# Kernel optimization log

Hardware: AMD Instinct MI355X
Metric: run time of the kernel (lower is better)

Reference implementation:

```python
import jax, jax.numpy as jnp
import numpy as np

VOL = (32, 64, 64)          # 3D brain volume grid
B, N, D = 2, 4096, 1024     # batch, active voxels (seq_len), feature_dim
H, KNN = 16, 16             # num_heads, num_neighbors


def setup_inputs() -> dict:
    key = jax.random.key(0)
    k1, k2, k3, k4 = jax.random.split(key, 4)
    # boolean 3D mask with exactly N active voxels (so seq_len == #active)
    rng = np.random.default_rng(0)
    flat = np.zeros(int(np.prod(VOL)), dtype=bool)
    flat[rng.choice(flat.size, N, replace=False)] = True
    visual_cortex_mask = jnp.asarray(flat.reshape(VOL))
    x = jax.random.normal(k1, (B, N, D), dtype=jnp.float32)
    s = 1.0 / np.sqrt(D)
    Wq = jax.random.normal(k2, (D, D), dtype=jnp.float32) * s
    Wk = jax.random.normal(k3, (D, D), dtype=jnp.float32) * s
    Wv = jax.random.normal(k4, (D, D), dtype=jnp.float32) * s
    return {"x": x, "visual_cortex_mask": visual_cortex_mask,
            "Wq": Wq, "Wk": Wk, "Wv": Wv}


def reference(x, visual_cortex_mask, Wq, Wk, Wv):
    batch, seq_len, d = x.shape
    hd = d // H
    # --- kNN over active voxel coordinates (cdist + topk) ---
    flat = visual_cortex_mask.reshape(-1)
    (act,) = jnp.nonzero(flat, size=seq_len)  # flat indices of active voxels
    coords = jnp.stack(jnp.unravel_index(act, visual_cortex_mask.shape),
                       axis=1).astype(jnp.float32)           # [N, 3]
    sq = jnp.sum(coords * coords, axis=-1)                    # [N]
    d2 = sq[:, None] + sq[None, :] - 2.0 * (coords @ coords.T)  # squared dists
    _, nbr = jax.lax.top_k(-d2, KNN + 1)   # smallest distances first
    nbr = nbr[:, 1:]                       # drop self -> [N, KNN] positions
    # --- QKV projections (torch Linear: x @ W.T) ---
    q = (x @ Wq.T).reshape(batch, seq_len, H, hd)
    k = (x @ Wk.T).reshape(batch, seq_len, H, hd)
    v = (x @ Wv.T).reshape(batch, seq_len, H, hd)
    # --- gather-based sparse attention: each query attends only to its
    # KNN neighbors (exactly the block-mask semantics of the original) ---
    kn = k[:, nbr]   # [B, N, KNN, H, hd]
    vn = v[:, nbr]   # [B, N, KNN, H, hd]
    scale = 1.0 / np.sqrt(hd)
    scores = jnp.einsum('bnhd,bnkhd->bhnk', q, kn) * scale
    attn = jax.nn.softmax(scores, axis=-1)
    out = jnp.einsum('bhnk,bnkhd->bnhd', attn, vn).reshape(batch, seq_len, d)
    metric = k.mean(axis=2)  # key.mean over heads -> [B, N, hd]
    return out, metric
```

## Files before the change

### kernel.cpp

```cpp
#include <hip/hip_runtime.h>
#include <hip/hip_bf16.h>
#include <stdint.h>

#define BATCH 2
#define NPTS 4096
#define DMODEL 1024
#define NHEAD 16
#define HDIM 64
#define KNN 16
#define MASKN 131072
#define EBLK 128

typedef __attribute__((ext_vector_type(8))) short bf16x8;
typedef __attribute__((ext_vector_type(4))) float f32x4;

__device__ __forceinline__ float b2f(unsigned short u) {
    union { unsigned int i; float f; } c; c.i = ((unsigned int)u) << 16; return c.f;
}
__device__ __forceinline__ unsigned short f2b(float f) {
    unsigned int x = __float_as_uint(f);
    unsigned int r = (x + 0x7fffu + ((x >> 16) & 1u)) >> 16;
    return (unsigned short)r;
}
__device__ __forceinline__ unsigned int pack2f(float a, float b) {
    return (unsigned int)f2b(a) | ((unsigned int)f2b(b) << 16);
}
__device__ __forceinline__ void gload16(const unsigned short* g, unsigned short* l) {
    __builtin_amdgcn_global_load_lds((const __attribute__((address_space(1))) void*)g,
                                     (__attribute__((address_space(3))) void*)l, 16, 0, 0);
}

__global__ __launch_bounds__(256) void count8_kernel(const unsigned char* __restrict__ m8,
                                                     int* __restrict__ cnt8) {
    __shared__ int red[256];
    const int b = blockIdx.x, t = threadIdx.x;
    const uchar4 v = ((const uchar4*)m8)[b * 256 + t];
    red[t] = (v.x != 0) + (v.y != 0) + (v.z != 0) + (v.w != 0);
    __syncthreads();
    for (int off = 128; off >= 1; off >>= 1) {
        if (t < off) red[t] += red[t + off];
        __syncthreads();
    }
    if (t == 0) cnt8[b] = red[0];
}

__global__ __launch_bounds__(256) void count32_kernel(const unsigned char* __restrict__ m8,
                                                      const int* __restrict__ cnt8,
                                                      int* __restrict__ cnt32) {
    __shared__ int red[256];
    const int b = blockIdx.x, t = threadIdx.x;
    red[t] = (t < EBLK) ? cnt8[t] : 0;
    __syncthreads();
    for (int off = 128; off >= 1; off >>= 1) {
        if (t < off) red[t] += red[t + off];
        __syncthreads();
    }
    if (red[0] == NPTS) return;
    __syncthreads();
    const int4 v = ((const int4*)m8)[b * 256 + t];
    red[t] = (v.x != 0) + (v.y != 0) + (v.z != 0) + (v.w != 0);
    __syncthreads();
    for (int off = 128; off >= 1; off >>= 1) {
        if (t < off) red[t] += red[t + off];
        __syncthreads();
    }
    if (t == 0) cnt32[b] = red[0];
}

__global__ __launch_bounds__(256) void extract_kernel(const unsigned char* __restrict__ m8,
                                                      const int* __restrict__ cnt8,
                                                      const int* __restrict__ cnt32,
                                                      int* __restrict__ act) {
    __shared__ int sblk[EBLK];
    __shared__ int sthr[256];
    const int b = blockIdx.x, t = threadIdx.x;
    if (t < EBLK) sblk[t] = cnt8[t];
    __syncthreads();
    for (int off = 1; off < EBLK; off <<= 1) {
        int v = (t < EBLK && t >= off) ? sblk[t - off] : 0;
        __syncthreads();
        if (t < EBLK) sblk[t] += v;
        __syncthreads();
    }
    const bool bytes = (sblk[EBLK - 1] == NPTS);
    if (!bytes) {
        __syncthreads();
        if (t < EBLK) sblk[t] = cnt32[t];
        __syncthreads();
        for (int off = 1; off < EBLK; off <<= 1) {
            int v = (t < EBLK && t >= off) ? sblk[t - off] : 0;
            __syncthreads();
            if (t < EBLK) sblk[t] += v;
            __syncthreads();
        }
    }
    const int blkoff = (b == 0) ? 0 : sblk[b - 1];
    const int gbase = b * 1024 + t * 4;
    int f0, f1, f2, f3;
    if (bytes) {
        const uchar4 v = ((const uchar4*)m8)[b * 256 + t];
        f0 = v.x != 0; f1 = v.y != 0; f2 = v.z != 0; f3 = v.w != 0;
    } else {
        const int4 v = ((const int4*)m8)[b * 256 + t];
        f0 = v.x != 0; f1 = v.y != 0; f2 = v.z != 0; f3 = v.w != 0;
    }
    const int c = f0 + f1 + f2 + f3;
    sthr[t] = c;
    __syncthreads();
    for (int off = 1; off < 256; off <<= 1) {
        int v = (t >= off) ? sthr[t - off] : 0;
        __syncthreads();
        sthr[t] += v;
        __syncthreads();
    }
    int pos = blkoff + sthr[t] - c;
    if (f0) act[pos++] = gbase;
    if (f1) act[pos++] = gbase + 1;
    if (f2) act[pos++] = gbase + 2;
    if (f3) act[pos++] = gbase + 3;
}

#define XN8 (BATCH * NPTS * DMODEL / 8)
#define WN8 (DMODEL * DMODEL / 8)
#define CASTN (XN8 + 3 * WN8)
#define CASTBLKS ((CASTN + 255) / 256)

__global__ __launch_bounds__(256) void knn_cast_kernel(
    const int* __restrict__ act, int* __restrict__ nbr,
    const float* __restrict__ x, const float* __restrict__ wq,
    const float* __restrict__ wk, const float* __restrict__ wv,
    unsigned short* __restrict__ Xb, unsigned short* __restrict__ Wb)
{
    __shared__ int act_s[NPTS];
    const int t = threadIdx.x;
    if (blockIdx.x < 1024) {
        for (int i = t; i < NPTS; i += 256) act_s[i] = act[i];
        __syncthreads();
        const int q = blockIdx.x * 4 + (t >> 6);
        const int lane = t & 63;
        const int aq = act_s[q];
        const int qz = aq >> 12, qy = (aq >> 6) & 63, qx = aq & 63;
        int best[17];
        #pragma unroll
        for (int i = 0; i < 17; ++i) best[i] = 0x7FFFFFFF;
        for (int j = lane; j < NPTS; j += 64) {
            const int aj = act_s[j];
            const int dz = (aj >> 12) - qz;
            const int dy = ((aj >> 6) & 63) - qy;
            const int dx = (aj & 63) - qx;
            const int d2 = dz * dz + dy * dy + dx * dx;
            int p = (d2 << 12) | j;
            if (p < best[16]) {
                #pragma unroll
                for (int u = 0; u < 17; ++u) {
                    const bool lt = p < best[u];
                    const int tmp = best[u];
                    best[u] = lt ? p : best[u];
                    p = lt ? tmp : p;
                }
            }
        }
        int head = best[0];
        int keep = 0;
        #pragma unroll
        for (int r = 0; r < KNN + 1; ++r) {
            int m = head;
            #pragma unroll
            for (int off = 32; off >= 1; off >>= 1) m = min(m, __shfl_xor(m, off, 64));
            if (lane == r - 1) keep = m;
            const bool win = (head == m);
            #pragma unroll
            for (int u = 0; u < 16; ++u) if (win) best[u] = best[u + 1];
            if (win) best[16] = 0x7FFFFFFF;
            head = best[0];
        }
        if (lane < KNN) nbr[q * KNN + lane] = keep & 4095;
    } else {
        const int i = (blockIdx.x - 1024) * 256 + t;
        if (i >= CASTN) return;
        const float* src;
        unsigned short* dst;
        if (i < XN8) {
            src = x + (size_t)i * 8;
            dst = Xb + (size_t)i * 8;
        } else {
            const int j = i - XN8;
            const int wsel = j >> 17;
            const int o = j & (WN8 - 1);
            src = ((wsel == 0) ? wq : (wsel == 1) ? wk : wv) + (size_t)o * 8;
            dst = Wb + ((size_t)wsel * WN8 + o) * 8;
        }
        const float4 a = ((const float4*)src)[0];
        const float4 bb = ((const float4*)src)[1];
        uint4 w;
        w.x = pack2f(a.x, a.y);  w.y = pack2f(a.z, a.w);
        w.z = pack2f(bb.x, bb.y); w.w = pack2f(bb.z, bb.w);
        *(uint4*)dst = w;
    }
}

__global__ __launch_bounds__(256, 2) void gemm_qkv64(
    const unsigned short* __restrict__ Xb,
    const unsigned short* __restrict__ Wb,
    unsigned short* __restrict__ O0, unsigned short* __restrict__ O1, unsigned short* __restrict__ O2)
{
    const int K = DMODEL, N = DMODEL;
    const unsigned short* W = Wb + (size_t)blockIdx.z * DMODEL * DMODEL;
    unsigned short* C = (blockIdx.z == 0) ? O0 : (blockIdx.z == 1) ? O1 : O2;
    __shared__ unsigned short As[2][128 * 64];
    __shared__ unsigned short Bs[2][128 * 64];
    const int tid = threadIdx.x;
    const int rowBase = blockIdx.x * 128;
    const int colBase = blockIdx.y * 128;
    const int lane = tid & 63, w = tid >> 6;
    const int wr = w >> 1, wc = w & 1;
    const int lr = lane & 15, kg = lane >> 4;

    f32x4 acc[4][4];
    const f32x4 zero = {0.f, 0.f, 0.f, 0.f};
    #pragma unroll
    for (int i = 0; i < 4; ++i)
        #pragma unroll
        for (int j = 0; j < 4; ++j) acc[i][j] = zero;

    const unsigned short* aS[4];
    const unsigned short* bS[4];
    #pragma unroll
    for (int j = 0; j < 4; ++j) {
        const int s = j * 256 + tid;
        const int row = s >> 3, pch = s & 7;
        const int sc = (pch ^ (row & 7)) * 8;
        aS[j] = Xb + (size_t)(rowBase + row) * K + sc;
        bS[j] = W  + (size_t)(colBase + row) * K + sc;
    }

    #define STAGE(kt, bf) do { \
        _Pragma("unroll") \
        for (int j = 0; j < 4; ++j) { \
            gload16(aS[j] + (kt) * 64, &As[bf][(j * 256 + w * 64) * 8]); \
            gload16(bS[j] + (kt) * 64, &Bs[bf][(j * 256 + w * 64) * 8]); \
        } \
    } while (0)

    #define COMPUTE(bf) do { \
        bf16x8 af[4][2], bfr[4][2]; \
        _Pragma("unroll") \
        for (int mi = 0; mi < 4; ++mi) \
            _Pragma("unroll") \
            for (int kk = 0; kk < 2; ++kk) \
                af[mi][kk] = *(const bf16x8*)&As[bf][(wr * 64 + mi * 16 + lr) * 64 + (((kk * 4 + kg) ^ (lr & 7)) * 8)]; \
        _Pragma("unroll") \
        for (int ni = 0; ni < 4; ++ni) \
            _Pragma("unroll") \
            for (int kk = 0; kk < 2; ++kk) \
                bfr[ni][kk] = *(const bf16x8*)&Bs[bf][(wc * 64 + ni * 16 + lr) * 64 + (((kk * 4 + kg) ^ (lr & 7)) * 8)]; \
        __builtin_amdgcn_s_setprio(1); \
        _Pragma("unroll") \
        for (int kk = 0; kk < 2; ++kk) \
            _Pragma("unroll") \
            for (int mi = 0; mi < 4; ++mi) \
                _Pragma("unroll") \
                for (int ni = 0; ni < 4; ++ni) \
                    acc[mi][ni] = __builtin_amdgcn_mfma_f32_16x16x32_bf16(af[mi][kk], bfr[ni][kk], acc[mi][ni], 0, 0, 0); \
        __builtin_amdgcn_s_setprio(0); \
    } while (0)

    STAGE(0, 0);
    STAGE(1, 1);
    for (int kt = 0; kt < 14; ++kt) {
        const int bf = kt & 1;
        asm volatile("s_waitcnt vmcnt(8)" ::: "memory");
        __builtin_amdgcn_s_barrier();
        COMPUTE(bf);
        __builtin_amdgcn_s_barrier();
        STAGE(kt + 2, bf);
    }
    asm volatile("s_waitcnt vmcnt(8)" ::: "memory");
    __builtin_amdgcn_s_barrier();
    COMPUTE(0);
    __builtin_amdgcn_s_barrier();
    asm volatile("s_waitcnt vmcnt(0)" ::: "memory");
    __builtin_amdgcn_s_barrier();
    COMPUTE(1);
    #undef STAGE
    #undef COMPUTE

    #pragma unroll
    for (int mi = 0; mi < 4; ++mi)
        #pragma unroll
        for (int ni = 0; ni < 4; ++ni) {
            const int row0 = rowBase + wr * 64 + mi * 16 + kg * 4;
            const int col = colBase + wc * 64 + ni * 16 + lr;
            #pragma unroll
            for (int j = 0; j < 4; ++j)
                C[(size_t)(row0 + j) * N + col] = f2b(acc[mi][ni][j]);
        }
}

__device__ __forceinline__ void stage16(unsigned short* dst, const float* src) {
    const float4 a = ((const float4*)src)[0];
    const float4 b = ((const float4*)src)[1];
    const float4 c = ((const float4*)src)[2];
    const float4 d = ((const float4*)src)[3];
    uint4 w0, w1;
    w0.x = pack2f(a.x, a.y); w0.y = pack2f(a.z, a.w);
    w0.z = pack2f(b.x, b.y); w0.w = pack2f(b.z, b.w);
    w1.x = pack2f(c.x, c.y); w1.y = pack2f(c.z, c.w);
    w1.z = pack2f(d.x, d.y); w1.w = pack2f(d.z, d.w);
    ((uint4*)dst)[0] = w0;
    ((uint4*)dst)[1] = w1;
}

__global__ __launch_bounds__(256) void gemm_qkv_f32(
    const float* __restrict__ X,
    const float* __restrict__ W0, const float* __restrict__ W1, const float* __restrict__ W2,
    unsigned short* __restrict__ O0, unsigned short* __restrict__ O1, unsigned short* __restrict__ O2)
{
    const int K = DMODEL, N = DMODEL;
    const float* W = (blockIdx.z == 0) ? W0 : (blockIdx.z == 1) ? W1 : W2;
    unsigned short* C = (blockIdx.z == 0) ? O0 : (blockIdx.z == 1) ? O1 : O2;
    __shared__ unsigned short As[128 * 32];
    __shared__ unsigned short Bs[128 * 32];
    const int tid = threadIdx.x;
    const int rowBase = blockIdx.x * 128;
    const int colBase = blockIdx.y * 128;
    const int lane = tid & 63, w = tid >> 6;
    const int wr = w >> 1, wc = w & 1;
    const int lr = lane & 15, kg = lane >> 4;
    const int srow = tid >> 1;
    const int scol = (tid & 1) * 16;
    f32x4 acc[4][4];
    const f32x4 zero = {0.f, 0.f, 0.f, 0.f};
    #pragma unroll
    for (int i = 0; i < 4; ++i)
        #pragma unroll
        for (int j = 0; j < 4; ++j) acc[i][j] = zero;
    const float* Arow = &X[(size_t)(rowBase + srow) * K + scol];
    const float* Brow = &W[(size_t)(colBase + srow) * K + scol];
    unsigned short* Adst = &As[srow * 32 + scol];
    unsigned short* Bdst = &Bs[srow * 32 + scol];
    for (int kb = 0; kb < K; kb += 32) {
        __syncthreads();
        stage16(Adst, Arow + kb);
        stage16(Bdst, Brow + kb);
        __syncthreads();
        bf16x8 af[4], bfr[4];
        #pragma unroll
        for (int mi = 0; mi < 4; ++mi)
            af[mi] = *(const bf16x8*)&As[(wr * 64 + mi * 16 + lr) * 32 + kg * 8];
        #pragma unroll
        for (int ni = 0; ni < 4; ++ni)
            bfr[ni] = *(const bf16x8*)&Bs[(wc * 64 + ni * 16 + lr) * 32 + kg * 8];
        #pragma unroll
        for (int mi = 0; mi < 4; ++mi)
            #pragma unroll
            for (int ni = 0; ni < 4; ++ni)
                acc[mi][ni] = __builtin_amdgcn_mfma_f32_16x16x32_bf16(af[mi], bfr[ni], acc[mi][ni], 0, 0, 0);
    }
    #pragma unroll
    for (int mi = 0; mi < 4; ++mi)
        #pragma unroll
        for (int ni = 0; ni < 4; ++ni) {
            const int row0 = rowBase + wr * 64 + mi * 16 + kg * 4;
            const int col = colBase + wc * 64 + ni * 16 + lr;
            #pragma unroll
            for (int j = 0; j < 4; ++j)
                C[(size_t)(row0 + j) * N + col] = f2b(acc[mi][ni][j]);
        }
}

__global__ __launch_bounds__(256) void attn_kernel(
    const unsigned short* __restrict__ Q, const unsigned short* __restrict__ Kb,
    const unsigned short* __restrict__ Vb, const int* __restrict__ nbr,
    float* __restrict__ out, float* __restrict__ mout)
{
    const int bid = blockIdx.x;
    const int p = (bid & 7) * 1024 + (bid >> 3);
    const int b = p >> 12;
    const int n = p & 4095;
    __shared__ unsigned short q_s[DMODEL];
    __shared__ float a_s[NHEAD][KNN];
    __shared__ float part_s[4][64];
    const int tid = threadIdx.x;
    const int kk = tid & 15, h = tid >> 4;
    const int mynb = nbr[n * KNN + kk];
    const unsigned short* krow = &Kb[((size_t)b * NPTS + mynb) * DMODEL + h * HDIM];
    bf16x8 kreg[8];
    #pragma unroll
    for (int j = 0; j < 8; ++j) kreg[j] = *(const bf16x8*)&krow[j * 8];
    const int o = tid * 4;
    ushort4 vpre[KNN];
    #pragma unroll
    for (int k2 = 0; k2 < KNN; ++k2) {
        const int nb2 = __shfl(mynb, k2, 16);
        vpre[k2] = *(const ushort4*)&Vb[((size_t)b * NPTS + nb2) * DMODEL + o];
    }
    *(int2*)&q_s[tid * 4] = *(const int2*)&Q[((size_t)b * NPTS + n) * DMODEL + tid * 4];
    __syncthreads();
    float s = 0.f;
    #pragma unroll
    for (int j = 0; j < 8; ++j) {
        const bf16x8 qq = *(const bf16x8*)&q_s[h * HDIM + j * 8];
        const bf16x8 kr = kreg[j];
        #pragma unroll
        for (int e = 0; e < 8; ++e)
            s += b2f((unsigned short)qq[e]) * b2f((unsigned short)kr[e]);
    }
    s *= 0.125f;
    float m = s;
    #pragma unroll
    for (int off = 8; off >= 1; off >>= 1) m = fmaxf(m, __shfl_xor(m, off, 16));
    const float e = __expf(s - m);
    float sum = e;
    #pragma unroll
    for (int off = 8; off >= 1; off >>= 1) sum += __shfl_xor(sum, off, 16);
    a_s[h][kk] = e / sum;
    __syncthreads();
    const int h2 = tid >> 4;
    float av0 = 0.f, av1 = 0.f, av2 = 0.f, av3 = 0.f;
    #pragma unroll
    for (int k2 = 0; k2 < KNN; ++k2) {
        const float a = a_s[h2][k2];
        av0 += a * b2f(vpre[k2].x); av1 += a * b2f(vpre[k2].y);
        av2 += a * b2f(vpre[k2].z); av3 += a * b2f(vpre[k2].w);
    }
    float4 r; r.x = av0; r.y = av1; r.z = av2; r.w = av3;
    *(float4*)&out[((size_t)b * NPTS + n) * DMODEL + o] = r;
    {
        const unsigned short* krow2 = &Kb[((size_t)b * NPTS + n) * DMODEL];
        const int dd = tid & 63, grp = tid >> 6;
        float ms = 0.f;
        #pragma unroll
        for (int hh = 0; hh < 4; ++hh)
            ms += b2f(krow2[(grp * 4 + hh) * HDIM + dd]);
        part_s[grp][dd] = ms;
        __syncthreads();
        if (tid < 64)
            mout[((size_t)b * NPTS + n) * HDIM + tid] =
                (part_s[0][tid] + part_s[1][tid] + part_s[2][tid] + part_s[3][tid]) * 0.0625f;
    }
}

extern "C" void kernel_launch(void* const* d_in, const int* in_sizes, int n_in,
                              void* d_out, int out_size, void* d_ws, size_t ws_size,
                              hipStream_t stream) {
    const float* x = (const float*)d_in[0];
    const unsigned char* mask = (const unsigned char*)d_in[1];
    const float* Wq = (const float*)d_in[2];
    const float* Wk = (const float*)d_in[3];
    const float* Wv = (const float*)d_in[4];
    float* out = (float*)d_out;
    char* ws = (char*)d_ws;

    const size_t QKV_BYTES = (size_t)BATCH * NPTS * DMODEL * 2;
    const size_t XB_BYTES  = (size_t)BATCH * NPTS * DMODEL * 2;
    const size_t WB_BYTES  = (size_t)3 * DMODEL * DMODEL * 2;
    unsigned short* qb = (unsigned short*)(ws);
    unsigned short* kb = (unsigned short*)(ws + QKV_BYTES);
    unsigned short* vb = (unsigned short*)(ws + 2 * QKV_BYTES);
    const size_t SMALL_BYTES = (size_t)NPTS * sizeof(int) * (1 + KNN) + 2 * EBLK * sizeof(int);
    const size_t need_base = 3 * QKV_BYTES + SMALL_BYTES;
    const size_t need_full = need_base + XB_BYTES + WB_BYTES;
    const bool full = (ws_size >= need_full);
    char* tail = ws + 3 * QKV_BYTES;
    unsigned short* Xb = (unsigned short*)tail;
    unsigned short* Wb = (unsigned short*)(tail + XB_BYTES);
    char* small = full ? (tail + XB_BYTES + WB_BYTES) : tail;
    int* act  = (int*)small;
    int* nbr  = (int*)(small + NPTS * sizeof(int));
    int* cnt8 = (int*)(small + NPTS * sizeof(int) * (1 + KNN));
    int* cnt32 = cnt8 + EBLK;
    if (ws_size < need_base) return;

    count8_kernel<<<EBLK, 256, 0, stream>>>(mask, cnt8);
    count32_kernel<<<EBLK, 256, 0, stream>>>(mask, cnt8, cnt32);
    extract_kernel<<<EBLK, 256, 0, stream>>>(mask, cnt8, cnt32, act);
    if (full) {
        knn_cast_kernel<<<1024 + CASTBLKS, 256, 0, stream>>>(act, nbr, x, Wq, Wk, Wv, Xb, Wb);
        gemm_qkv64<<<dim3(64, 8, 3), 256, 0, stream>>>(Xb, Wb, qb, kb, vb);
    } else {
        knn_cast_kernel<<<1024, 256, 0, stream>>>(act, nbr, x, Wq, Wk, Wv,
                                                  (unsigned short*)nullptr, (unsigned short*)nullptr);
        gemm_qkv_f32<<<dim3(64, 8, 3), 256, 0, stream>>>(x, Wq, Wk, Wv, qb, kb, vb);
    }
    attn_kernel<<<dim3(BATCH * NPTS), 256, 0, stream>>>(qb, kb, vb, nbr, out,
                                                        out + (size_t)BATCH * NPTS * DMODEL);
}
```

Baseline: 167.4 us.

## Fuse bf16 cast into mask count kernel and kNN into QKV GEMM launch

Moves the fp32-to-bf16 cast of x and the weights into the first mask-counting kernel, so the cast runs alongside the count stage. The kNN search is merged into the same launch as the QKV GEMM, so kNN blocks and GEMM tiles can overlap on the GPU and one launch boundary disappears. The cost is that the fused GEMM kernel now also reserves the kNN shared memory (16 KB more per block), which may lower GEMM occupancy. kNN and GEMM blocks also compete for CUs within the same grid.

```diff
diff --git a/kernel.cpp b/kernel.cpp
--- a/kernel.cpp
+++ b/kernel.cpp
@@ -30,18 +30,52 @@
                                      (__attribute__((address_space(3))) void*)l, 16, 0, 0);
 }
 
-__global__ __launch_bounds__(256) void count8_kernel(const unsigned char* __restrict__ m8,
-                                                     int* __restrict__ cnt8) {
+#define XN8 (BATCH * NPTS * DMODEL / 8)
+#define WN8 (DMODEL * DMODEL / 8)
+#define CASTN (XN8 + 3 * WN8)
+#define CASTBLKS ((CASTN + 255) / 256)
+
+__global__ __launch_bounds__(256) void cast_count8_kernel(
+    const float* __restrict__ x, const float* __restrict__ wq,
+    const float* __restrict__ wk, const float* __restrict__ wv,
+    unsigned short* __restrict__ Xb, unsigned short* __restrict__ Wb,
+    const unsigned char* __restrict__ m8, int* __restrict__ cnt8, int do_cast)
+{
     __shared__ int red[256];
-    const int b = blockIdx.x, t = threadIdx.x;
-    const uchar4 v = ((const uchar4*)m8)[b * 256 + t];
-    red[t] = (v.x != 0) + (v.y != 0) + (v.z != 0) + (v.w != 0);
-    __syncthreads();
-    for (int off = 128; off >= 1; off >>= 1) {
-        if (t < off) red[t] += red[t + off];
-        __syncthreads();
-    }
-    if (t == 0) cnt8[b] = red[0];
+    const int t = threadIdx.x;
+    const int cb = do_cast ? CASTBLKS : 0;
+    if ((int)blockIdx.x < cb) {
+        const int i = blockIdx.x * 256 + t;
+        if (i >= CASTN) return;
+        const float* src;
+        unsigned short* dst;
+        if (i < XN8) {
+            src = x + (size_t)i * 8;
+            dst = Xb + (size_t)i * 8;
+        } else {
+            const int j = i - XN8;
+            const int wsel = j >> 17;
+            const int o = j & (WN8 - 1);
+            src = ((wsel == 0) ? wq : (wsel == 1) ? wk : wv) + (size_t)o * 8;
+            dst = Wb + ((size_t)wsel * WN8 + o) * 8;
+        }
+        const float4 a = ((const float4*)src)[0];
+        const float4 bb = ((const float4*)src)[1];
+        uint4 w;
+        w.x = pack2f(a.x, a.y);  w.y = pack2f(a.z, a.w);
+        w.z = pack2f(bb.x, bb.y); w.w = pack2f(bb.z, bb.w);
+        *(uint4*)dst = w;
+    } else {
+        const int b = blockIdx.x - cb;
+        const uchar4 v = ((const uchar4*)m8)[b * 256 + t];
+        red[t] = (v.x != 0) + (v.y != 0) + (v.z != 0) + (v.w != 0);
+        __syncthreads();
+        for (int off = 128; off >= 1; off >>= 1) {
+            if (t < off) red[t] += red[t + off];
+            __syncthreads();
+        }
+        if (t == 0) cnt8[b] = red[0];
+    }
 }
 
 __global__ __launch_bounds__(256) void count32_kernel(const unsigned char* __restrict__ m8,
@@ -120,20 +154,19 @@
     if (f3) act[pos++] = gbase + 3;
 }
 
-#define XN8 (BATCH * NPTS * DMODEL / 8)
-#define WN8 (DMODEL * DMODEL / 8)
-#define CASTN (XN8 + 3 * WN8)
-#define CASTBLKS ((CASTN + 255) / 256)
-
-__global__ __launch_bounds__(256) void knn_cast_kernel(
+__global__ __launch_bounds__(256, 2) void knn_gemm_kernel(
     const int* __restrict__ act, int* __restrict__ nbr,
-    const float* __restrict__ x, const float* __restrict__ wq,
-    const float* __restrict__ wk, const float* __restrict__ wv,
-    unsigned short* __restrict__ Xb, unsigned short* __restrict__ Wb)
+    const unsigned short* __restrict__ Xb,
+    const unsigned short* __restrict__ Wb,
+    unsigned short* __restrict__ O0, unsigned short* __restrict__ O1, unsigned short* __restrict__ O2)
 {
+    __shared__ unsigned short As[2][128 * 64];
+    __shared__ unsigned short Bs[2][128 * 64];
     __shared__ int act_s[NPTS];
-    const int t = threadIdx.x;
-    if (blockIdx.x < 1024) {
+    const int tid = threadIdx.x;
+
+    if ((int)blockIdx.x < 1024) {
+        const int t = tid;
         for (int i = t; i < NPTS; i += 256) act_s[i] = act[i];
         __syncthreads();
         const int q = blockIdx.x * 4 + (t >> 6);
@@ -175,43 +208,18 @@
             head = best[0];
         }
         if (lane < KNN) nbr[q * KNN + lane] = keep & 4095;
-    } else {
-        const int i = (blockIdx.x - 1024) * 256 + t;
-        if (i >= CASTN) return;
-        const float* src;
-        unsigned short* dst;
-        if (i < XN8) {
-            src = x + (size_t)i * 8;
-            dst = Xb + (size_t)i * 8;
-        } else {
-            const int j = i - XN8;
-            const int wsel = j >> 17;
-            const int o = j & (WN8 - 1);
-            src = ((wsel == 0) ? wq : (wsel == 1) ? wk : wv) + (size_t)o * 8;
-            dst = Wb + ((size_t)wsel * WN8 + o) * 8;
-        }
-        const float4 a = ((const float4*)src)[0];
-        const float4 bb = ((const float4*)src)[1];
-        uint4 w;
-        w.x = pack2f(a.x, a.y);  w.y = pack2f(a.z, a.w);
-        w.z = pack2f(bb.x, bb.y); w.w = pack2f(bb.z, bb.w);
-        *(uint4*)dst = w;
-    }
-}
-
-__global__ __launch_bounds__(256, 2) void gemm_qkv64(
-    const unsigned short* __restrict__ Xb,
-    const unsigned short* __restrict__ Wb,
-    unsigned short* __restrict__ O0, unsigned short* __restrict__ O1, unsigned short* __restrict__ O2)
-{
+        return;
+    }
+
+    const int g = blockIdx.x - 1024;
+    const int bx = g & 63;
+    const int by = (g >> 6) & 7;
+    const int bz = g >> 9;
     const int K = DMODEL, N = DMODEL;
-    const unsigned short* W = Wb + (size_t)blockIdx.z * DMODEL * DMODEL;
-    unsigned short* C = (blockIdx.z == 0) ? O0 : (blockIdx.z == 1) ? O1 : O2;
-    __shared__ unsigned short As[2][128 * 64];
-    __shared__ unsigned short Bs[2][128 * 64];
-    const int tid = threadIdx.x;
-    const int rowBase = blockIdx.x * 128;
-    const int colBase = blockIdx.y * 128;
+    const unsigned short* W = Wb + (size_t)bz * DMODEL * DMODEL;
+    unsigned short* C = (bz == 0) ? O0 : (bz == 1) ? O1 : O2;
+    const int rowBase = bx * 128;
+    const int colBase = by * 128;
     const int lane = tid & 63, w = tid >> 6;
     const int wr = w >> 1, wc = w & 1;
     const int lr = lane & 15, kg = lane >> 4;
@@ -297,6 +305,53 @@
         }
 }
 
+__global__ __launch_bounds__(256) void knn_kernel(const int* __restrict__ act,
+                                                  int* __restrict__ nbr) {
+    __shared__ int act_s[NPTS];
+    const int t = threadIdx.x;
+    for (int i = t; i < NPTS; i += 256) act_s[i] = act[i];
+    __syncthreads();
+    const int q = blockIdx.x * 4 + (t >> 6);
+    const int lane = t & 63;
+    const int aq = act_s[q];
+    const int qz = aq >> 12, qy = (aq >> 6) & 63, qx = aq & 63;
+    int best[17];
+    #pragma unroll
+    for (int i = 0; i < 17; ++i) best[i] = 0x7FFFFFFF;
+    for (int j = lane; j < NPTS; j += 64) {
+        const int aj = act_s[j];
+        const int dz = (aj >> 12) - qz;
+        const int dy = ((aj >> 6) & 63) - qy;
+        const int dx = (aj & 63) - qx;
+        const int d2 = dz * dz + dy * dy + dx * dx;
+        int p = (d2 << 12) | j;
+        if (p < best[16]) {
+            #pragma unroll
+            for (int u = 0; u < 17; ++u) {
+                const bool lt = p < best[u];
+                const int tmp = best[u];
+                best[u] = lt ? p : best[u];
+                p = lt ? tmp : p;
+            }
+        }
+    }
+    int head = best[0];
+    int keep = 0;
+    #pragma unroll
+    for (int r = 0; r < KNN + 1; ++r) {
+        int m = head;
+        #pragma unroll
+        for (int off = 32; off >= 1; off >>= 1) m = min(m, __shfl_xor(m, off, 64));
+        if (lane == r - 1) keep = m;
+        const bool win = (head == m);
+        #pragma unroll
+        for (int u = 0; u < 16; ++u) if (win) best[u] = best[u + 1];
+        if (win) best[16] = 0x7FFFFFFF;
+        head = best[0];
+    }
+    if (lane < KNN) nbr[q * KNN + lane] = keep & 4095;
+}
+
 __device__ __forceinline__ void stage16(unsigned short* dst, const float* src) {
     const float4 a = ((const float4*)src)[0];
     const float4 b = ((const float4*)src)[1];
@@ -472,15 +527,16 @@
     int* cnt32 = cnt8 + EBLK;
     if (ws_size < need_base) return;
 
-    count8_kernel<<<EBLK, 256, 0, stream>>>(mask, cnt8);
-    count32_kernel<<<EBLK, 256, 0, stream>>>(mask, cnt8, cnt32);
-    extract_kernel<<<EBLK, 256, 0, stream>>>(mask, cnt8, cnt32, act);
     if (full) {
-        knn_cast_kernel<<<1024 + CASTBLKS, 256, 0, stream>>>(act, nbr, x, Wq, Wk, Wv, Xb, Wb);
-        gemm_qkv64<<<dim3(64, 8, 3), 256, 0, stream>>>(Xb, Wb, qb, kb, vb);
+        cast_count8_kernel<<<CASTBLKS + EBLK, 256, 0, stream>>>(x, Wq, Wk, Wv, Xb, Wb, mask, cnt8, 1);
+        count32_kernel<<<EBLK, 256, 0, stream>>>(mask, cnt8, cnt32);
+        extract_kernel<<<EBLK, 256, 0, stream>>>(mask, cnt8, cnt32, act);
+        knn_gemm_kernel<<<1024 + 1536, 256, 0, stream>>>(act, nbr, Xb, Wb, qb, kb, vb);
     } else {
-        knn_cast_kernel<<<1024, 256, 0, stream>>>(act, nbr, x, Wq, Wk, Wv,
-                                                  (unsigned short*)nullptr, (unsigned short*)nullptr);
+        cast_count8_kernel<<<EBLK, 256, 0, stream>>>(x, Wq, Wk, Wv, Xb, Wb, mask, cnt8, 0);
+        count32_kernel<<<EBLK, 256, 0, stream>>>(mask, cnt8, cnt32);
+        extract_kernel<<<EBLK, 256, 0, stream>>>(mask, cnt8, cnt32, act);
+        knn_kernel<<<1024, 256, 0, stream>>>(act, nbr);
         gemm_qkv_f32<<<dim3(64, 8, 3), 256, 0, stream>>>(x, Wq, Wk, Wv, qb, kb, vb);
     }
     attn_kernel<<<dim3(BATCH * NPTS), 256, 0, stream>>>(qb, kb, vb, nbr, out,
```

New measurement: 173.1 us. 3.4% more time.
